# Optimization experiments

Measured on AMD Instinct MI355X. Metric: run time of the kernel, lower is better.

The kernel has to match this reference:

```python
import jax, jax.numpy as jnp
import numpy as np

B, S, K = 256, 2048, 64


def setup_inputs() -> dict:
    key = jax.random.key(0)
    k1, k2, k3, k4, k5 = jax.random.split(key, 5)
    return {
        "scores": jax.random.normal(k1, (B, S, K), dtype=jnp.float32),
        "states": jax.random.randint(k2, (B, S), 0, K),
        "transition": jax.random.normal(k3, (K, K), dtype=jnp.float32),
        "source": jax.random.uniform(k4, (K,), dtype=jnp.float32),
        "sink": jax.random.uniform(k5, (K,), dtype=jnp.float32),
    }


def _log_partition(scores, transition, source, sink):
    # alpha_0[b,j] = source[j] + scores[b,0,j]
    alpha0 = source[None, :] + scores[:, 0, :]

    def step(alpha, s_t):  # alpha: [B,K], s_t: [B,K]
        # tmp[b,i,j] = alpha[b,i] + transition[i,j] + scores[b,t,j]
        tmp = alpha[:, :, None] + transition[None, :, :] + s_t[:, None, :]
        return jax.nn.logsumexp(tmp, axis=1), None

    alpha, _ = jax.lax.scan(step, alpha0, jnp.swapaxes(scores[:, 1:], 0, 1))
    return jax.nn.logsumexp(alpha + sink[None, :], axis=1)  # [B]


def _log_score(scores, states, transition, source, sink):
    # emission scores along the gold path
    emit = jnp.take_along_axis(scores, states[:, :, None], axis=2)[:, :, 0].sum(axis=1)
    # transition scores between consecutive gold tags
    trans = transition[states[:, :-1], states[:, 1:]].sum(axis=1)
    return source[states[:, 0]] + emit + trans + sink[states[:, -1]]  # [B]


def reference(scores, states, transition, source, sink):
    # neg_log_likelihood: mean over batch of logZ - gold path score
    losses = _log_partition(scores, transition, source, sink) - _log_score(
        scores, states, transition, source, sink
    )
    return losses.mean()
```

## Files before the change

kernel.cpp:

```cpp
#include <hip/hip_runtime.h>
#include <math.h>

#define CRF_B 256
#define CRF_S 2048
#define CRF_K 64
#define NSEG 64
#define BURN 32
#define DEPTH 64

typedef short bf16x8 __attribute__((ext_vector_type(8)));
typedef float f32x4 __attribute__((ext_vector_type(4)));


__device__ __forceinline__ void lds_fence() { asm volatile("" ::: "memory"); }

__device__ __forceinline__ unsigned bf16rne(float x) {
    unsigned u = __float_as_uint(x);
    return (u + 0x7FFFu + ((u >> 16) & 1u)) >> 16;
}
__device__ __forceinline__ unsigned pktrunc(float x, float y) {
    return __builtin_amdgcn_perm(__float_as_uint(y), __float_as_uint(x), 0x07060302u);
}
__device__ __forceinline__ int expOf(float m) {
    return ((__float_as_int(m) >> 23) & 255) - 126;
}

__global__ __launch_bounds__(256, 1) void crf_scan(
    const float* __restrict__ scores, const int* __restrict__ states,
    const float* __restrict__ trans, const float* __restrict__ source,
    const float* __restrict__ sink, float* __restrict__ ws)
{
    const int tid = threadIdx.x;
    const int lane = tid & 63;
    const int w = tid >> 6;
    const int b = blockIdx.x;
    const int c = lane & 15;
    const int q = lane >> 4;
    const int s = w * 16 + c;

    float* wsC = ws;
    float* wsV = ws + CRF_B * NSEG;
    float* wsG = wsV + CRF_B * CRF_K;

    __shared__ __align__(16) short Pbuf[4][16 * 72];
    short* myP = Pbuf[w];

    const float* scb = scores + (size_t)b * CRF_S * CRF_K;

    {
        const int* st = states + b * CRF_S;
        float g = 0.f;
#pragma unroll
        for (int it = 0; it < 8; ++it) {
            int p = w * 512 + it * 64 + lane;
            int cur = st[p];
            g += scb[(size_t)p * CRF_K + cur];
            if (p > 0) g += trans[st[p - 1] * CRF_K + cur];
            if (p == 0) g += source[cur];
            if (p == CRF_S - 1) g += sink[cur];
        }
#pragma unroll
        for (int m = 32; m >= 1; m >>= 1) g += __shfl_xor(g, m, 64);
        if (lane == 0) wsG[b * 4 + w] = g;
    }

    bf16x8 Af[4][2];
#pragma unroll
    for (int g4 = 0; g4 < 4; ++g4)
#pragma unroll
        for (int h = 0; h < 2; ++h) {
            bf16x8 t;
#pragma unroll
            for (int jv = 0; jv < 8; ++jv)
                t[jv] = (short)bf16rne(__expf(trans[(h * 32 + q * 8 + jv) * CRF_K + g4 * 16 + c]));
            Af[g4][h] = t;
        }

    float ini[16];
#pragma unroll
    for (int i = 0; i < 16; ++i) {
        int st8 = 16 * (i >> 2) + 4 * q + (i & 3);
        ini[i] = __expf(source[st8] + scb[st8]);
    }

#pragma unroll
    for (int g4 = 0; g4 < 4; ++g4)
        *(int2*)(myP + c * 72 + 16 * g4 + 4 * q) =
            make_int2((int)0x3F803F80u, (int)0x3F803F80u);
    lds_fence();
    bf16x8 bf0 = *(const bf16x8*)(myP + c * 72 + q * 8);
    bf16x8 bf1 = *(const bf16x8*)(myP + c * 72 + 32 + q * 8);

    float4 raw4[4][4];
    const float* scq = scb + 4 * q;
    auto ld4 = [&](int k) {
        int t = s * 32 - 32 + k;
        t = min(max(t, 0), CRF_S - 1);
        const float* pr = scq + (size_t)t * CRF_K;
        const int sl = k & 3;
#pragma unroll
        for (int g4 = 0; g4 < 4; ++g4)
            raw4[sl][g4] = *(const float4*)(pr + 16 * g4);
    };
#pragma unroll
    for (int k = 0; k < 4; ++k) ld4(k);

    float v[16];
    int cint = 0, e_pend = 0;

    for (int kk = 0; kk < DEPTH; kk += 4) {
#pragma unroll
        for (int ph = 0; ph < 4; ++ph) {
            const int k = kk + ph;
            float es[16];
#pragma unroll
            for (int g4 = 0; g4 < 4; ++g4) {
                const float4 r4 = raw4[ph][g4];
                es[g4 * 4 + 0] = __expf(r4.x);
                es[g4 * 4 + 1] = __expf(r4.y);
                es[g4 * 4 + 2] = __expf(r4.z);
                es[g4 * 4 + 3] = __expf(r4.w);
            }
            f32x4 acc[4];
#pragma unroll
            for (int g4 = 0; g4 < 4; ++g4) {
                f32x4 z = {0.f, 0.f, 0.f, 0.f};
                z = __builtin_amdgcn_mfma_f32_16x16x32_bf16(Af[g4][0], bf0, z, 0, 0, 0);
                z = __builtin_amdgcn_mfma_f32_16x16x32_bf16(Af[g4][1], bf1, z, 0, 0, 0);
                acc[g4] = z;
            }
            if (ph == 0) {
                const float s2 = ldexpf(1.0f, -e_pend);
                cint += e_pend;
#pragma unroll
                for (int i = 0; i < 16; ++i) v[i] = acc[i >> 2][i & 3] * es[i] * s2;
            } else {
#pragma unroll
                for (int i = 0; i < 16; ++i) v[i] = acc[i >> 2][i & 3] * es[i];
            }
            if (k == BURN - 1) {
                float mc = v[0];
#pragma unroll
                for (int i = 1; i < 16; ++i) mc = fmaxf(mc, v[i]);
                mc = fmaxf(mc, __shfl_xor(mc, 16, 64));
                mc = fmaxf(mc, __shfl_xor(mc, 32, 64));
                const float sc2 = ldexpf(1.0f, -expOf(mc));
#pragma unroll
                for (int i = 0; i < 16; ++i) v[i] *= sc2;
                cint = 0;
                e_pend = 0;
            }
            if (k == BURN) {
                if (s == 0) {
#pragma unroll
                    for (int i = 0; i < 16; ++i) v[i] = ini[i];
                }
                float mc = v[0];
#pragma unroll
                for (int i = 1; i < 16; ++i) mc = fmaxf(mc, v[i]);
                mc = fmaxf(mc, __shfl_xor(mc, 16, 64));
                mc = fmaxf(mc, __shfl_xor(mc, 32, 64));
                const int ec = expOf(mc);
                if (s == 0) {
                    const float sc2 = ldexpf(1.0f, -ec);
#pragma unroll
                    for (int i = 0; i < 16; ++i) v[i] *= sc2;
                    cint = ec;
                }
            }
            if (ph == 3 && k != BURN - 1) {
                float mx = v[0];
#pragma unroll
                for (int i = 1; i < 16; ++i) mx = fmaxf(mx, v[i]);
                mx = fmaxf(mx, __shfl_xor(mx, 16, 64));
                mx = fmaxf(mx, __shfl_xor(mx, 32, 64));
                e_pend = expOf(mx);
            }
#pragma unroll
            for (int g4 = 0; g4 < 4; ++g4) {
                unsigned lo = pktrunc(v[g4 * 4 + 0], v[g4 * 4 + 1]);
                unsigned hi = pktrunc(v[g4 * 4 + 2], v[g4 * 4 + 3]);
                *(int2*)(myP + c * 72 + 16 * g4 + 4 * q) = make_int2((int)lo, (int)hi);
            }
            lds_fence();
            bf0 = *(const bf16x8*)(myP + c * 72 + q * 8);
            bf1 = *(const bf16x8*)(myP + c * 72 + 32 + q * 8);
            ld4(k + 4);
        }
    }

    float mf = v[0];
#pragma unroll
    for (int i = 1; i < 16; ++i) mf = fmaxf(mf, v[i]);
    mf = fmaxf(mf, __shfl_xor(mf, 16, 64));
    mf = fmaxf(mf, __shfl_xor(mf, 32, 64));
    const int ef = expOf(mf);
    cint += ef;
    const float sf = ldexpf(1.0f, -ef);

    if (q == 0) wsC[b * NSEG + s] = (float)cint * 0.6931471805599453f;
    if (s == NSEG - 1) {
#pragma unroll
        for (int i = 0; i < 16; ++i)
            wsV[b * CRF_K + 16 * (i >> 2) + 4 * q + (i & 3)] = v[i] * sf;
    }
}

__global__ __launch_bounds__(256) void crf_finish(
    const float* __restrict__ ws, const float* __restrict__ sink,
    float* __restrict__ out)
{
    const int b = threadIdx.x;
    const float* wsC = ws;
    const float* wsV = ws + CRF_B * NSEG;
    const float* wsG = wsV + CRF_B * CRF_K;

    __shared__ float esink[CRF_K];
    if (b < CRF_K) esink[b] = __expf(sink[b]);
    __syncthreads();

    float cs = 0.f;
#pragma unroll 8
    for (int s = 0; s < NSEG; ++s) cs += wsC[b * NSEG + s];
    float dot = 0.f;
#pragma unroll 8
    for (int j = 0; j < CRF_K; ++j) dot += wsV[b * CRF_K + j] * esink[j];
    float gold = wsG[b * 4 + 0] + wsG[b * 4 + 1] + wsG[b * 4 + 2] + wsG[b * 4 + 3];
    float loss = cs + logf(dot) - gold;

    __shared__ float red[256];
    red[b] = loss;
    __syncthreads();
    for (int s2 = 128; s2 > 0; s2 >>= 1) {
        if (b < s2) red[b] += red[b + s2];
        __syncthreads();
    }
    if (b == 0) out[0] = red[0] * (1.0f / CRF_B);
}

extern "C" void kernel_launch(void* const* d_in, const int* in_sizes, int n_in,
                              void* d_out, int out_size, void* d_ws, size_t ws_size,
                              hipStream_t stream) {
    const float* scores = (const float*)d_in[0];
    const int*   states = (const int*)d_in[1];
    const float* trans  = (const float*)d_in[2];
    const float* source = (const float*)d_in[3];
    const float* sink   = (const float*)d_in[4];

    float* ws = (float*)d_ws;
    float* out = (float*)d_out;

    crf_scan<<<CRF_B, 256, 0, stream>>>(scores, states, trans, source, sink, ws);
    crf_finish<<<1, 256, 0, stream>>>(ws, sink, out);
}
```

Measured before the change: 228.5 us.

## Double segment count with 512-thread blocks and fold per-batch loss into scan

Splits each sequence into 128 segments of length 16 (burn-in 16, depth 32) handled by 8 waves per block instead of 64 segments of 32. Each wave's serial MFMA recurrence chain is halved, which shortens the critical path. The price is more redundant burn-in work overall and a shorter burn-in that may hurt convergence accuracy. It also moves the per-batch reduction (segment log-scale sum, sink dot product, gold score) into the scan kernel via shared memory, so the finish kernel only averages the losses.

```diff
diff --git a/kernel.cpp b/kernel.cpp
--- a/kernel.cpp
+++ b/kernel.cpp
@@ -4,13 +4,13 @@
 #define CRF_B 256
 #define CRF_S 2048
 #define CRF_K 64
-#define NSEG 64
-#define BURN 32
-#define DEPTH 64
+#define NSEG 128
+#define SEGL 16
+#define BURN 16
+#define DEPTH 32
 
 typedef short bf16x8 __attribute__((ext_vector_type(8)));
 typedef float f32x4 __attribute__((ext_vector_type(4)));
-
 
 __device__ __forceinline__ void lds_fence() { asm volatile("" ::: "memory"); }
 
@@ -25,10 +25,10 @@
     return ((__float_as_int(m) >> 23) & 255) - 126;
 }
 
-__global__ __launch_bounds__(256, 1) void crf_scan(
+__global__ __launch_bounds__(512, 2) void crf_scan(
     const float* __restrict__ scores, const int* __restrict__ states,
     const float* __restrict__ trans, const float* __restrict__ source,
-    const float* __restrict__ sink, float* __restrict__ ws)
+    const float* __restrict__ sink, float* __restrict__ lossOut)
 {
     const int tid = threadIdx.x;
     const int lane = tid & 63;
@@ -38,11 +38,10 @@
     const int q = lane >> 4;
     const int s = w * 16 + c;
 
-    float* wsC = ws;
-    float* wsV = ws + CRF_B * NSEG;
-    float* wsG = wsV + CRF_B * CRF_K;
-
-    __shared__ __align__(16) short Pbuf[4][16 * 72];
+    __shared__ __align__(16) short Pbuf[8][16 * 72];
+    __shared__ float sC[NSEG];
+    __shared__ float gW[8];
+    __shared__ float dotSh;
     short* myP = Pbuf[w];
 
     const float* scb = scores + (size_t)b * CRF_S * CRF_K;
@@ -51,8 +50,8 @@
         const int* st = states + b * CRF_S;
         float g = 0.f;
 #pragma unroll
-        for (int it = 0; it < 8; ++it) {
-            int p = w * 512 + it * 64 + lane;
+        for (int it = 0; it < 4; ++it) {
+            int p = w * 256 + it * 64 + lane;
             int cur = st[p];
             g += scb[(size_t)p * CRF_K + cur];
             if (p > 0) g += trans[st[p - 1] * CRF_K + cur];
@@ -61,7 +60,7 @@
         }
 #pragma unroll
         for (int m = 32; m >= 1; m >>= 1) g += __shfl_xor(g, m, 64);
-        if (lane == 0) wsG[b * 4 + w] = g;
+        if (lane == 0) gW[w] = g;
     }
 
     bf16x8 Af[4][2];
@@ -94,7 +93,7 @@
     float4 raw4[4][4];
     const float* scq = scb + 4 * q;
     auto ld4 = [&](int k) {
-        int t = s * 32 - 32 + k;
+        int t = s * SEGL - BURN + k;
         t = min(max(t, 0), CRF_S - 1);
         const float* pr = scq + (size_t)t * CRF_K;
         const int sl = k & 3;
@@ -198,38 +197,40 @@
     cint += ef;
     const float sf = ldexpf(1.0f, -ef);
 
-    if (q == 0) wsC[b * NSEG + s] = (float)cint * 0.6931471805599453f;
-    if (s == NSEG - 1) {
-#pragma unroll
-        for (int i = 0; i < 16; ++i)
-            wsV[b * CRF_K + 16 * (i >> 2) + 4 * q + (i & 3)] = v[i] * sf;
+    if (q == 0) sC[s] = (float)cint * 0.6931471805599453f;
+    if (w == 7) {
+        float pd = 0.f;
+        if (c == 15) {
+#pragma unroll
+            for (int i = 0; i < 16; ++i) {
+                int st8 = 16 * (i >> 2) + 4 * q + (i & 3);
+                pd += v[i] * sf * __expf(sink[st8]);
+            }
+        }
+        pd += __shfl_xor(pd, 16, 64);
+        pd += __shfl_xor(pd, 32, 64);
+        if (lane == 15) dotSh = pd;
+    }
+    __syncthreads();
+    if (w == 0) {
+        float t2 = sC[lane] + sC[lane + 64];
+#pragma unroll
+        for (int m = 32; m >= 1; m >>= 1) t2 += __shfl_xor(t2, m, 64);
+        if (lane == 0) {
+            float gold = 0.f;
+#pragma unroll
+            for (int i = 0; i < 8; ++i) gold += gW[i];
+            lossOut[b] = t2 + logf(dotSh) - gold;
+        }
     }
 }
 
 __global__ __launch_bounds__(256) void crf_finish(
-    const float* __restrict__ ws, const float* __restrict__ sink,
-    float* __restrict__ out)
+    const float* __restrict__ loss, float* __restrict__ out)
 {
     const int b = threadIdx.x;
-    const float* wsC = ws;
-    const float* wsV = ws + CRF_B * NSEG;
-    const float* wsG = wsV + CRF_B * CRF_K;
-
-    __shared__ float esink[CRF_K];
-    if (b < CRF_K) esink[b] = __expf(sink[b]);
-    __syncthreads();
-
-    float cs = 0.f;
-#pragma unroll 8
-    for (int s = 0; s < NSEG; ++s) cs += wsC[b * NSEG + s];
-    float dot = 0.f;
-#pragma unroll 8
-    for (int j = 0; j < CRF_K; ++j) dot += wsV[b * CRF_K + j] * esink[j];
-    float gold = wsG[b * 4 + 0] + wsG[b * 4 + 1] + wsG[b * 4 + 2] + wsG[b * 4 + 3];
-    float loss = cs + logf(dot) - gold;
-
     __shared__ float red[256];
-    red[b] = loss;
+    red[b] = loss[b];
     __syncthreads();
     for (int s2 = 128; s2 > 0; s2 >>= 1) {
         if (b < s2) red[b] += red[b + s2];
@@ -247,9 +248,9 @@
     const float* source = (const float*)d_in[3];
     const float* sink   = (const float*)d_in[4];
 
-    float* ws = (float*)d_ws;
+    float* loss = (float*)d_ws;
     float* out = (float*)d_out;
 
-    crf_scan<<<CRF_B, 256, 0, stream>>>(scores, states, trans, source, sink, ws);
-    crf_finish<<<1, 256, 0, stream>>>(ws, sink, out);
-}
+    crf_scan<<<CRF_B, 512, 0, stream>>>(scores, states, trans, source, sink, loss);
+    crf_finish<<<1, 256, 0, stream>>>(loss, out);
+}
```

Measured after the change: 221.0 us. -3.3%, faster.
